# Kernel tuning notes

Hardware: AMD Instinct MI355X
Metric: run time of the kernel (lower is better)

## Reference

```python
import jax, jax.numpy as jnp
import numpy as np

B = 4096      # batch
D = 64        # state_dim
H = 512       # hidden_dim


def setup_inputs() -> dict:
    key = jax.random.key(0)
    ks = jax.random.split(key, 16)

    def init(k, shape, fan_in):
        return jax.random.normal(k, shape, dtype=jnp.float32) / np.float32(np.sqrt(fan_in))

    mu = jax.random.normal(ks[0], (B, D), dtype=jnp.float32)
    sigma_diag = 0.1 * jax.random.uniform(ks[1], (B, D), dtype=jnp.float32) + 0.01
    states = jnp.concatenate([mu, sigma_diag], axis=1)  # [B, 2D]

    return {
        "t": jnp.float32(0.5),
        "states": states,
        # dynamics net: tanh MLP D -> H -> H -> D
        "W1": init(ks[2], (H, D), D), "b1": jnp.zeros((H,), jnp.float32),
        "W2": init(ks[3], (H, H), H), "b2": jnp.zeros((H,), jnp.float32),
        "W3": init(ks[4], (D, H), H), "b3": jnp.zeros((D,), jnp.float32),
        # process-noise net: tanh MLP D -> H -> H -> D, softplus head (diagonal Q)
        "V1": init(ks[5], (H, D), D), "c1": jnp.zeros((H,), jnp.float32),
        "V2": init(ks[6], (H, H), H), "c2": jnp.zeros((H,), jnp.float32),
        "V3": init(ks[7], (D, H), H), "c3": jnp.zeros((D,), jnp.float32),
    }


def reference(t, states, W1, b1, W2, b2, W3, b3, V1, c1, V2, c2, V3, c3):
    # UPN ODE function, diagonal-covariance path.
    mu = states[:, :D]          # [B, D]
    sigma_diag = states[:, D:]  # [B, D]

    # dynamics MLP forward (t is an autonomous-system placeholder, unused)
    h1 = jnp.tanh(mu @ W1.T + b1)   # [B, H]
    h2 = jnp.tanh(h1 @ W2.T + b2)   # [B, H]
    mu_drift = h2 @ W3.T + b3       # [B, D]

    # analytic batched Jacobian of the tanh MLP: J = W3 diag(1-h2^2) W2 diag(1-h1^2) W1
    d1 = 1.0 - h1 * h1              # [B, H]
    d2 = 1.0 - h2 * h2              # [B, H]
    inner = jnp.einsum('hk,bk,kd->bhd', W2, d1, W1)   # [B, H, D]
    J = jnp.einsum('oh,bh,bhd->bod', W3, d2, inner)   # [B, D, D]
    J_diag = jnp.diagonal(J, axis1=1, axis2=2)        # [B, D]

    # process-noise net: diagonal Q, softplus ensures positivity
    g1 = jnp.tanh(mu @ V1.T + c1)
    g2 = jnp.tanh(g1 @ V2.T + c2)
    Q_diag = jax.nn.softplus(g2 @ V3.T + c3)          # [B, D]

    sigma_drift = 2.0 * J_diag * sigma_diag + Q_diag  # [B, D]
    return jnp.concatenate([mu_drift, sigma_drift], axis=1)  # [B, 2D]
```

## Files before the change

### kernel.cpp

```cpp
#include <hip/hip_runtime.h>
#include <hip/hip_bf16.h>

#define BB 4096
#define DD 64
#define HH 512

typedef __hip_bfloat16 bf16;
typedef _Float16 f16;
typedef __attribute__((ext_vector_type(8))) short bf16x8;
typedef __attribute__((ext_vector_type(8))) _Float16 f16x8;
typedef __attribute__((ext_vector_type(4))) float f32x4;

__device__ __forceinline__ float bf2f(bf16 x) { return __bfloat162float(x); }
__device__ __forceinline__ float u16tof(unsigned short u) {
  union { unsigned int i; float f; } v; v.i = ((unsigned int)u) << 16; return v.f;
}
#define BC8(p) __builtin_bit_cast(bf16x8, *(const uint4*)(p))
#define BCH8(p) __builtin_bit_cast(f16x8, *(const uint4*)(p))


__global__ __launch_bounds__(256) void cvt_weights(
    const float* __restrict__ W2, const float* __restrict__ V2,
    const float* __restrict__ W1, const float* __restrict__ V1,
    const float* __restrict__ W3, const float* __restrict__ V3,
    bf16* __restrict__ W2bf, bf16* __restrict__ V2bf, f16* __restrict__ W1Th,
    bf16* __restrict__ W1bf, bf16* __restrict__ V1bf,
    bf16* __restrict__ W3bf, bf16* __restrict__ V3bf, f16* __restrict__ W2h) {
  int blk = blockIdx.x, t = threadIdx.x;
  if (blk < 512) {
    const float* src = (blk < 256) ? W2 : V2;
    bf16* dst = (blk < 256) ? W2bf : V2bf;
    int i = ((blk & 255) * 256 + t) * 4;
    float4 v = *(const float4*)(src + i);
    bf16 o[4] = {__float2bfloat16(v.x), __float2bfloat16(v.y),
                 __float2bfloat16(v.z), __float2bfloat16(v.w)};
    *(uint2*)(dst + i) = *(uint2*)o;
  } else if (blk < 544) {
    int e = (blk - 512) * 1024 + t * 4;
    int d = e >> 9, k0 = e & 511;
    f16 o[4];
#pragma unroll
    for (int j = 0; j < 4; ++j) o[j] = (f16)W1[(size_t)(k0 + j) * 64 + d];
    *(uint2*)(W1Th + e) = *(uint2*)o;
  } else if (blk < 672) {
    int which = (blk - 544) >> 5;
    int local = (blk - 544) & 31;
    const float* src = (which == 0) ? W1 : (which == 1) ? V1 : (which == 2) ? W3 : V3;
    bf16* dst = (which == 0) ? W1bf : (which == 1) ? V1bf : (which == 2) ? W3bf : V3bf;
    int i = (local * 256 + t) * 4;
    float4 v = *(const float4*)(src + i);
    bf16 o[4] = {__float2bfloat16(v.x), __float2bfloat16(v.y),
                 __float2bfloat16(v.z), __float2bfloat16(v.w)};
    *(uint2*)(dst + i) = *(uint2*)o;
  } else {
    int i = ((blk - 672) * 256 + t) * 4;
    float4 v = *(const float4*)(W2 + i);
    f16 o[4] = {(f16)v.x, (f16)v.y, (f16)v.z, (f16)v.w};
    *(uint2*)(W2h + i) = *(uint2*)o;
  }
}

__global__ __launch_bounds__(256) void fwd(
    const float* __restrict__ states,
    const bf16* __restrict__ W1bf, const float* __restrict__ b1,
    const bf16* __restrict__ W2bf, const float* __restrict__ b2,
    const bf16* __restrict__ W3bf, const float* __restrict__ b3,
    const bf16* __restrict__ V1bf, const float* __restrict__ c1,
    const bf16* __restrict__ V2bf, const float* __restrict__ c2,
    const bf16* __restrict__ V3bf, const float* __restrict__ c3,
    bf16* __restrict__ Xbf, bf16* __restrict__ Ybf, float* __restrict__ out) {
  __shared__ __align__(16) bf16 mus[16 * 72];
  __shared__ __align__(16) bf16 Xres[16 * 520];
  __shared__ __align__(16) bf16 Bs[128 * 72];
  __shared__ __align__(16) bf16 Ych[16 * 136];
  const int bt = blockIdx.x * 16;
  const int path = blockIdx.y;
  const bf16* Wa = path ? V1bf : W1bf;
  const float* ba = path ? c1 : b1;
  const bf16* Wb = path ? V2bf : W2bf;
  const float* bbv = path ? c2 : b2;
  const bf16* Wc = path ? V3bf : W3bf;
  const float* bcv = path ? c3 : b3;
  const int t = threadIdx.x;
  const int lane = t & 63;
  const int w = t >> 6;
  const int c = lane & 15, q = lane >> 4;

  if (t < 128) {
    int row = t >> 3, cg = (t & 7) * 8;
    bf16 o[8];
#pragma unroll
    for (int j = 0; j < 8; j += 4) {
      float4 v = *(const float4*)(states + (size_t)(bt + row) * 128 + cg + j);
      o[j] = __float2bfloat16(v.x); o[j + 1] = __float2bfloat16(v.y);
      o[j + 2] = __float2bfloat16(v.z); o[j + 3] = __float2bfloat16(v.w);
    }
    *(uint4*)(mus + row * 72 + cg) = *(const uint4*)o;
  }
  __syncthreads();

  for (int nch = 0; nch < 4; ++nch) {
    if (nch) __syncthreads();
#pragma unroll
    for (int i = 0; i < 4; ++i) {
      int g = t + i * 256;
      int row = g >> 3, kb = (g & 7) * 8;
      *(uint4*)(Bs + row * 72 + kb) =
          *(const uint4*)(Wa + (size_t)(nch * 128 + row) * 64 + kb);
    }
    __syncthreads();
    f32x4 acc1[2] = {};
#pragma unroll
    for (int s = 0; s < 2; ++s) {
      bf16x8 af = BC8(mus + c * 72 + s * 32 + q * 8);
#pragma unroll
      for (int nt = 0; nt < 2; ++nt) {
        bf16x8 bfr = BC8(Bs + (w * 32 + nt * 16 + c) * 72 + s * 32 + q * 8);
        acc1[nt] = __builtin_amdgcn_mfma_f32_16x16x32_bf16(af, bfr, acc1[nt], 0, 0, 0);
      }
    }
#pragma unroll
    for (int nt = 0; nt < 2; ++nt) {
      int col = nch * 128 + w * 32 + nt * 16 + c;
      float bias = ba[col];
#pragma unroll
      for (int r = 0; r < 4; ++r) {
        int row = q * 4 + r;
        float x = tanhf(acc1[nt][r] + bias);
        Xres[row * 520 + col] = __float2bfloat16(x);
        if (!path) Xbf[(size_t)(bt + row) * HH + col] = __float2bfloat16(x);
      }
    }
  }
  __syncthreads();

  f32x4 acc3 = {};
  for (int hch = 0; hch < 4; ++hch) {
    f32x4 acc2[2] = {};
    for (int kc = 0; kc < 8; ++kc) {
      __syncthreads();
#pragma unroll
      for (int i = 0; i < 4; ++i) {
        int g = t + i * 256;
        int row = g >> 3, kb = (g & 7) * 8;
        *(uint4*)(Bs + row * 72 + kb) =
            *(const uint4*)(Wb + (size_t)(hch * 128 + row) * HH + kc * 64 + kb);
      }
      __syncthreads();
#pragma unroll
      for (int s = 0; s < 2; ++s) {
        bf16x8 af = BC8(Xres + c * 520 + kc * 64 + s * 32 + q * 8);
#pragma unroll
        for (int nt = 0; nt < 2; ++nt) {
          bf16x8 bfr = BC8(Bs + (w * 32 + nt * 16 + c) * 72 + s * 32 + q * 8);
          acc2[nt] = __builtin_amdgcn_mfma_f32_16x16x32_bf16(af, bfr, acc2[nt], 0, 0, 0);
        }
      }
    }
    __syncthreads();
#pragma unroll
    for (int nt = 0; nt < 2; ++nt) {
      int hl = w * 32 + nt * 16 + c;
      int h = hch * 128 + hl;
      float bias = bbv[h];
#pragma unroll
      for (int r = 0; r < 4; ++r) {
        int row = q * 4 + r;
        float y = tanhf(acc2[nt][r] + bias);
        Ych[row * 136 + hl] = __float2bfloat16(y);
        if (!path) Ybf[(size_t)(bt + row) * HH + h] = __float2bfloat16(y);
      }
    }
    __syncthreads();
#pragma unroll
    for (int s3 = 0; s3 < 4; ++s3) {
      bf16x8 bf3 = BC8(Wc + (size_t)(w * 16 + c) * HH + hch * 128 + s3 * 32 + q * 8);
      bf16x8 af3 = BC8(Ych + c * 136 + s3 * 32 + q * 8);
      acc3 = __builtin_amdgcn_mfma_f32_16x16x32_bf16(af3, bf3, acc3, 0, 0, 0);
    }
  }
  {
    int o = w * 16 + c;
    float bias = bcv[o];
#pragma unroll
    for (int r = 0; r < 4; ++r) {
      int row = q * 4 + r;
      float v = acc3[r] + bias;
      if (path) {
        v = fmaxf(v, 0.0f) + log1pf(expf(-fabsf(v)));
        out[(size_t)(bt + row) * 128 + 64 + o] = v;
      } else {
        out[(size_t)(bt + row) * 128 + o] = v;
      }
    }
  }
}

__global__ __launch_bounds__(256, 4) void k4_gemm(
    const bf16* __restrict__ Xbf, const bf16* __restrict__ Ybf,
    const f16* __restrict__ W1Th, const f16* __restrict__ W2h,
    const float* __restrict__ W3, float* __restrict__ Jpart) {
  __shared__ __align__(16) f16 smem[2 * 128 * 72];
  __shared__ __align__(16) f16 d1h[2 * 512];
  __shared__ __align__(16) float d2f[2 * 128];
  f16* As = smem;
  f16* Bs = smem + 128 * 72;
  const int bt = blockIdx.x;
  const int h0 = blockIdx.y * 128;
  const int t = threadIdx.x;
  const int lane = t & 63;
  const int w = t >> 6, wm = w & 1, wn = w >> 1;
  const int c = lane & 15, q = lane >> 4;

#pragma unroll
  for (int i = 0; i < 4; ++i) {
    int e = t + i * 256;
    float x = bf2f(Xbf[(size_t)(bt * 2 + (e >> 9)) * HH + (e & 511)]);
    d1h[e] = (f16)(1.0f - x * x);
  }
  {
    float y = bf2f(Ybf[(size_t)(bt * 2 + (t >> 7)) * HH + h0 + (t & 127)]);
    d2f[t] = 1.0f - y * y;
  }
  __syncthreads();

  f32x4 acc[4][4] = {};
  for (int kc = 0; kc < 8; ++kc) {
#pragma unroll
    for (int i = 0; i < 4; ++i) {
      int g = t + i * 256;
      int m = g >> 3, kb = (g & 7) * 8;
      int bb = m >> 6, dl = m & 63;
      f16x8 w1v = BCH8(W1Th + (size_t)dl * HH + kc * 64 + kb);
      f16x8 d1v = BCH8(d1h + bb * 512 + kc * 64 + kb);
      f16x8 av = d1v * w1v;
      *(uint4*)(As + m * 72 + kb) = __builtin_bit_cast(uint4, av);
      *(uint4*)(Bs + m * 72 + kb) =
          *(const uint4*)(W2h + (size_t)(h0 + m) * HH + kc * 64 + kb);
    }
    __syncthreads();
#pragma unroll
    for (int s = 0; s < 2; ++s) {
      f16x8 af[4], bfr[4];
#pragma unroll
      for (int mt = 0; mt < 4; ++mt)
        af[mt] = BCH8(As + (wm * 64 + mt * 16 + c) * 72 + s * 32 + q * 8);
#pragma unroll
      for (int nt = 0; nt < 4; ++nt)
        bfr[nt] = BCH8(Bs + (wn * 64 + nt * 16 + c) * 72 + s * 32 + q * 8);
#pragma unroll
      for (int mt = 0; mt < 4; ++mt)
#pragma unroll
        for (int nt = 0; nt < 4; ++nt)
          acc[mt][nt] = __builtin_amdgcn_mfma_f32_16x16x32_f16(
              af[mt], bfr[nt], acc[mt][nt], 0, 0, 0);
    }
    __syncthreads();
  }

  f16* w3s = As;
  float* red = (float*)Bs;
#pragma unroll
  for (int i = 0; i < 8; ++i) {
    int e = (t + i * 256) * 4;
    int dl = e >> 7, hl = e & 127;
    float4 v = *(const float4*)(W3 + (size_t)dl * HH + h0 + hl);
    f16 o[4] = {(f16)v.x, (f16)v.y, (f16)v.z, (f16)v.w};
    *(uint2*)(w3s + dl * 136 + hl) = *(uint2*)o;
  }
  __syncthreads();

#pragma unroll
  for (int mt = 0; mt < 4; ++mt) {
#pragma unroll
    for (int r = 0; r < 4; ++r) {
      int m = wm * 64 + mt * 16 + q * 4 + r;
      int bb = m >> 6, dl = m & 63;
      float v = 0.f;
#pragma unroll
      for (int nt = 0; nt < 4; ++nt) {
        int n = wn * 64 + nt * 16 + c;
        v += acc[mt][nt][r] * d2f[bb * 128 + n] * (float)w3s[dl * 136 + n];
      }
      v += __shfl_xor(v, 1);
      v += __shfl_xor(v, 2);
      v += __shfl_xor(v, 4);
      v += __shfl_xor(v, 8);
      if (c == 0) red[wn * 128 + m] = v;
    }
  }
  __syncthreads();
  if (t < 128) {
    float J = red[t] + red[128 + t];
    Jpart[(size_t)blockIdx.y * (BB * 64) + (size_t)bt * 128 + t] = J;
  }
}

__global__ __launch_bounds__(256) void combine(
    const float* __restrict__ Jpart, const float* __restrict__ states,
    float* __restrict__ out) {
  int idx = blockIdx.x * 256 + threadIdx.x;
  int b = idx >> 6, d = idx & 63;
  const int plane = BB * 64;
  float J = Jpart[idx] + Jpart[plane + idx] + Jpart[2 * plane + idx] +
            Jpart[3 * plane + idx];
  float sig = states[(size_t)b * 128 + 64 + d];
  float qd = out[(size_t)b * 128 + 64 + d];
  out[(size_t)b * 128 + 64 + d] = 2.0f * J * sig + qd;
}

extern "C" void kernel_launch(void* const* d_in, const int* in_sizes, int n_in,
                              void* d_out, int out_size, void* d_ws, size_t ws_size,
                              hipStream_t stream) {
  const float* states = (const float*)d_in[1];
  const float* W1 = (const float*)d_in[2];
  const float* b1 = (const float*)d_in[3];
  const float* W2 = (const float*)d_in[4];
  const float* b2 = (const float*)d_in[5];
  const float* W3 = (const float*)d_in[6];
  const float* b3 = (const float*)d_in[7];
  const float* V1 = (const float*)d_in[8];
  const float* c1 = (const float*)d_in[9];
  const float* V2 = (const float*)d_in[10];
  const float* c2 = (const float*)d_in[11];
  const float* V3 = (const float*)d_in[12];
  const float* c3 = (const float*)d_in[13];
  float* out = (float*)d_out;

  bf16* Xbf = (bf16*)d_ws;
  bf16* Ybf = Xbf + (size_t)BB * HH;
  bf16* W2bf = Ybf + (size_t)BB * HH;
  bf16* V2bf = W2bf + (size_t)HH * HH;
  bf16* W1bf = V2bf + (size_t)HH * HH;
  bf16* V1bf = W1bf + (size_t)HH * DD;
  bf16* W3bf = V1bf + (size_t)HH * DD;
  bf16* V3bf = W3bf + (size_t)DD * HH;
  f16* W1Th = (f16*)(V3bf + (size_t)DD * HH);
  f16* W2h = W1Th + (size_t)DD * HH;
  float* Jpart = (float*)(W2h + (size_t)HH * HH);

  cvt_weights<<<dim3(928), 256, 0, stream>>>(W2, V2, W1, V1, W3, V3,
                                             W2bf, V2bf, W1Th, W1bf, V1bf,
                                             W3bf, V3bf, W2h);
  fwd<<<dim3(256, 2), 256, 0, stream>>>(states, W1bf, b1, W2bf, b2, W3bf, b3,
                                        V1bf, c1, V2bf, c2, V3bf, c3,
                                        Xbf, Ybf, out);
  k4_gemm<<<dim3(2048, 4), 256, 0, stream>>>(Xbf, Ybf, W1Th, W2h, W3, Jpart);
  combine<<<dim3(1024), 256, 0, stream>>>(Jpart, states, out);
}
```

Measured before the change: 316.3 us.

## Loop over hidden chunks in-block and fuse combine into Jacobian kernel

```diff
diff --git a/kernel.cpp b/kernel.cpp
--- a/kernel.cpp
+++ b/kernel.cpp
@@ -199,14 +199,14 @@
 __global__ __launch_bounds__(256, 4) void k4_gemm(
     const bf16* __restrict__ Xbf, const bf16* __restrict__ Ybf,
     const f16* __restrict__ W1Th, const f16* __restrict__ W2h,
-    const float* __restrict__ W3, float* __restrict__ Jpart) {
+    const float* __restrict__ W3, const float* __restrict__ states,
+    float* __restrict__ out) {
   __shared__ __align__(16) f16 smem[2 * 128 * 72];
   __shared__ __align__(16) f16 d1h[2 * 512];
   __shared__ __align__(16) float d2f[2 * 128];
   f16* As = smem;
   f16* Bs = smem + 128 * 72;
   const int bt = blockIdx.x;
-  const int h0 = blockIdx.y * 128;
   const int t = threadIdx.x;
   const int lane = t & 63;
   const int w = t >> 6, wm = w & 1, wn = w >> 1;
@@ -218,95 +218,97 @@
     float x = bf2f(Xbf[(size_t)(bt * 2 + (e >> 9)) * HH + (e & 511)]);
     d1h[e] = (f16)(1.0f - x * x);
   }
-  {
-    float y = bf2f(Ybf[(size_t)(bt * 2 + (t >> 7)) * HH + h0 + (t & 127)]);
-    d2f[t] = 1.0f - y * y;
-  }
   __syncthreads();
 
-  f32x4 acc[4][4] = {};
-  for (int kc = 0; kc < 8; ++kc) {
-#pragma unroll
-    for (int i = 0; i < 4; ++i) {
-      int g = t + i * 256;
-      int m = g >> 3, kb = (g & 7) * 8;
-      int bb = m >> 6, dl = m & 63;
-      f16x8 w1v = BCH8(W1Th + (size_t)dl * HH + kc * 64 + kb);
-      f16x8 d1v = BCH8(d1h + bb * 512 + kc * 64 + kb);
-      f16x8 av = d1v * w1v;
-      *(uint4*)(As + m * 72 + kb) = __builtin_bit_cast(uint4, av);
-      *(uint4*)(Bs + m * 72 + kb) =
-          *(const uint4*)(W2h + (size_t)(h0 + m) * HH + kc * 64 + kb);
-    }
-    __syncthreads();
-#pragma unroll
-    for (int s = 0; s < 2; ++s) {
-      f16x8 af[4], bfr[4];
-#pragma unroll
-      for (int mt = 0; mt < 4; ++mt)
-        af[mt] = BCH8(As + (wm * 64 + mt * 16 + c) * 72 + s * 32 + q * 8);
-#pragma unroll
-      for (int nt = 0; nt < 4; ++nt)
-        bfr[nt] = BCH8(Bs + (wn * 64 + nt * 16 + c) * 72 + s * 32 + q * 8);
-#pragma unroll
-      for (int mt = 0; mt < 4; ++mt)
+  float jp[4][4] = {};
+  for (int hp = 0; hp < 4; ++hp) {
+    const int h0 = hp * 128;
+    f32x4 acc[4][4] = {};
+    for (int kc = 0; kc < 8; ++kc) {
+#pragma unroll
+      for (int i = 0; i < 4; ++i) {
+        int g = t + i * 256;
+        int m = g >> 3, kb = (g & 7) * 8;
+        int bb = m >> 6, dl = m & 63;
+        f16x8 w1v = BCH8(W1Th + (size_t)dl * HH + kc * 64 + kb);
+        f16x8 d1v = BCH8(d1h + bb * 512 + kc * 64 + kb);
+        f16x8 av = d1v * w1v;
+        *(uint4*)(As + m * 72 + kb) = __builtin_bit_cast(uint4, av);
+        *(uint4*)(Bs + m * 72 + kb) =
+            *(const uint4*)(W2h + (size_t)(h0 + m) * HH + kc * 64 + kb);
+      }
+      if (kc == 0) {
+        float y = bf2f(Ybf[(size_t)(bt * 2 + (t >> 7)) * HH + h0 + (t & 127)]);
+        d2f[t] = 1.0f - y * y;
+      }
+      __syncthreads();
+#pragma unroll
+      for (int s = 0; s < 2; ++s) {
+        f16x8 af[4], bfr[4];
+#pragma unroll
+        for (int mt = 0; mt < 4; ++mt)
+          af[mt] = BCH8(As + (wm * 64 + mt * 16 + c) * 72 + s * 32 + q * 8);
 #pragma unroll
         for (int nt = 0; nt < 4; ++nt)
-          acc[mt][nt] = __builtin_amdgcn_mfma_f32_16x16x32_f16(
-              af[mt], bfr[nt], acc[mt][nt], 0, 0, 0);
-    }
-    __syncthreads();
-  }
-
-  f16* w3s = As;
+          bfr[nt] = BCH8(Bs + (wn * 64 + nt * 16 + c) * 72 + s * 32 + q * 8);
+#pragma unroll
+        for (int mt = 0; mt < 4; ++mt)
+#pragma unroll
+          for (int nt = 0; nt < 4; ++nt)
+            acc[mt][nt] = __builtin_amdgcn_mfma_f32_16x16x32_f16(
+                af[mt], bfr[nt], acc[mt][nt], 0, 0, 0);
+      }
+      __syncthreads();
+    }
+
+    f16* w3s = As;
+#pragma unroll
+    for (int i = 0; i < 8; ++i) {
+      int e = (t + i * 256) * 4;
+      int dl = e >> 7, hl = e & 127;
+      float4 v = *(const float4*)(W3 + (size_t)dl * HH + h0 + hl);
+      f16 o[4] = {(f16)v.x, (f16)v.y, (f16)v.z, (f16)v.w};
+      *(uint2*)(w3s + dl * 136 + hl) = *(uint2*)o;
+    }
+    __syncthreads();
+#pragma unroll
+    for (int mt = 0; mt < 4; ++mt) {
+#pragma unroll
+      for (int r = 0; r < 4; ++r) {
+        int m = wm * 64 + mt * 16 + q * 4 + r;
+        int bb = m >> 6, dl = m & 63;
+        float v = 0.f;
+#pragma unroll
+        for (int nt = 0; nt < 4; ++nt) {
+          int n = wn * 64 + nt * 16 + c;
+          v += acc[mt][nt][r] * d2f[bb * 128 + n] * (float)w3s[dl * 136 + n];
+        }
+        jp[mt][r] += v;
+      }
+    }
+    __syncthreads();
+  }
+
   float* red = (float*)Bs;
 #pragma unroll
-  for (int i = 0; i < 8; ++i) {
-    int e = (t + i * 256) * 4;
-    int dl = e >> 7, hl = e & 127;
-    float4 v = *(const float4*)(W3 + (size_t)dl * HH + h0 + hl);
-    f16 o[4] = {(f16)v.x, (f16)v.y, (f16)v.z, (f16)v.w};
-    *(uint2*)(w3s + dl * 136 + hl) = *(uint2*)o;
-  }
-  __syncthreads();
-
-#pragma unroll
-  for (int mt = 0; mt < 4; ++mt) {
+  for (int mt = 0; mt < 4; ++mt)
 #pragma unroll
     for (int r = 0; r < 4; ++r) {
-      int m = wm * 64 + mt * 16 + q * 4 + r;
-      int bb = m >> 6, dl = m & 63;
-      float v = 0.f;
-#pragma unroll
-      for (int nt = 0; nt < 4; ++nt) {
-        int n = wn * 64 + nt * 16 + c;
-        v += acc[mt][nt][r] * d2f[bb * 128 + n] * (float)w3s[dl * 136 + n];
-      }
+      float v = jp[mt][r];
       v += __shfl_xor(v, 1);
       v += __shfl_xor(v, 2);
       v += __shfl_xor(v, 4);
       v += __shfl_xor(v, 8);
-      if (c == 0) red[wn * 128 + m] = v;
-    }
-  }
+      if (c == 0) red[wn * 128 + wm * 64 + mt * 16 + q * 4 + r] = v;
+    }
   __syncthreads();
   if (t < 128) {
     float J = red[t] + red[128 + t];
-    Jpart[(size_t)blockIdx.y * (BB * 64) + (size_t)bt * 128 + t] = J;
-  }
-}
-
-__global__ __launch_bounds__(256) void combine(
-    const float* __restrict__ Jpart, const float* __restrict__ states,
-    float* __restrict__ out) {
-  int idx = blockIdx.x * 256 + threadIdx.x;
-  int b = idx >> 6, d = idx & 63;
-  const int plane = BB * 64;
-  float J = Jpart[idx] + Jpart[plane + idx] + Jpart[2 * plane + idx] +
-            Jpart[3 * plane + idx];
-  float sig = states[(size_t)b * 128 + 64 + d];
-  float qd = out[(size_t)b * 128 + 64 + d];
-  out[(size_t)b * 128 + 64 + d] = 2.0f * J * sig + qd;
+    int bl = bt * 2 + (t >> 6), d = t & 63;
+    float sig = states[(size_t)bl * 128 + 64 + d];
+    float qd = out[(size_t)bl * 128 + 64 + d];
+    out[(size_t)bl * 128 + 64 + d] = 2.0f * J * sig + qd;
+  }
 }
 
 extern "C" void kernel_launch(void* const* d_in, const int* in_sizes, int n_in,
@@ -337,7 +339,6 @@
   bf16* V3bf = W3bf + (size_t)DD * HH;
   f16* W1Th = (f16*)(V3bf + (size_t)DD * HH);
   f16* W2h = W1Th + (size_t)DD * HH;
-  float* Jpart = (float*)(W2h + (size_t)HH * HH);
 
   cvt_weights<<<dim3(928), 256, 0, stream>>>(W2, V2, W1, V1, W3, V3,
                                              W2bf, V2bf, W1Th, W1bf, V1bf,
@@ -345,6 +346,5 @@
   fwd<<<dim3(256, 2), 256, 0, stream>>>(states, W1bf, b1, W2bf, b2, W3bf, b3,
                                         V1bf, c1, V2bf, c2, V3bf, c3,
                                         Xbf, Ybf, out);
-  k4_gemm<<<dim3(2048, 4), 256, 0, stream>>>(Xbf, Ybf, W1Th, W2h, W3, Jpart);
-  combine<<<dim3(1024), 256, 0, stream>>>(Jpart, states, out);
-}
+  k4_gemm<<<dim3(2048), 256, 0, stream>>>(Xbf, Ybf, W1Th, W2h, W3, states, out);
+}
```

Result: slower. 471.4 us (+49.0%).
